# Optimization experiments

Measured on AMD Instinct MI355X. Metric: run time of the kernel, lower is better.

Reference implementation:

```python
import jax, jax.numpy as jnp
import numpy as np

B, C, D, H, W = 8, 256, 128, 64, 64


def setup_inputs() -> dict:
    key = jax.random.key(0)
    ks = jax.random.split(key, 7)
    s = 1.0 / np.sqrt(C)
    return {
        "q": jax.random.normal(ks[0], (B, C, H, W), dtype=jnp.float32),
        "k": jax.random.normal(ks[1], (B, C, H, W), dtype=jnp.float32),
        "v": jax.random.normal(ks[2], (B, C, H, W), dtype=jnp.float32),
        "W_theta": jax.random.normal(ks[3], (D, C), dtype=jnp.float32) * s,
        "W_phi": jax.random.normal(ks[4], (D, C), dtype=jnp.float32) * s,
        "W_g": jax.random.normal(ks[5], (D, C), dtype=jnp.float32) * s,
        "W_out": jax.random.normal(ks[6], (C, D), dtype=jnp.float32) * (1.0 / np.sqrt(D)),
    }


def reference(q, k, v, W_theta, W_phi, W_g, W_out):
    # 1x1 conv projections (no bias) == channel matmuls
    b, c, h, w = q.shape
    d = W_theta.shape[0]
    n = h * w
    qp = jnp.einsum('bchw,dc->bhwd', q, W_theta).reshape(b, n, d)   # [B,N,d]
    kp = jnp.einsum('bchw,dc->bhwd', k, W_phi).reshape(b, n, d)     # [B,N,d]
    vp = jnp.einsum('bchw,dc->bhwd', v, W_g).reshape(b, n, d)       # [B,N,d]
    # embedded_gaussian: scores / sqrt(d), softmax over dim=1 (query axis!)
    scores = jnp.einsum('bnd,bmd->bnm', qp, kp) / jnp.sqrt(jnp.asarray(d, qp.dtype))
    attn = jax.nn.softmax(scores, axis=1)                           # NOTE: axis=1, matches torch dim=1
    out = jnp.einsum('bnm,bmd->bnd', attn, vp).reshape(b, h, w, d)  # [B,H,W,d]
    out = jnp.einsum('bhwd,cd->bchw', out, W_out)                   # conv_out 1x1
    return v + out
```

## Files before the change

### kernel.cpp

```cpp
#include <hip/hip_runtime.h>
#include <stdint.h>

#define B_ 8
#define C_ 256
#define D_ 128
#define N_ 4096

typedef __bf16 bf16x8 __attribute__((ext_vector_type(8)));
typedef uint16_t u16x8 __attribute__((ext_vector_type(8)));
typedef uint16_t u16x4 __attribute__((ext_vector_type(4)));
typedef float f32x4 __attribute__((ext_vector_type(4)));

__device__ inline uint16_t f2bf(float x) {
    union { float f; uint32_t u; } v; v.f = x;
    uint32_t u = v.u;
    return (uint16_t)((u + 0x7FFFu + ((u >> 16) & 1u)) >> 16);
}

__global__ __launch_bounds__(256) void prep_weights(
    const float* __restrict__ wt, const float* __restrict__ wp,
    const float* __restrict__ wg, const float* __restrict__ wo,
    uint16_t* __restrict__ bwt, uint16_t* __restrict__ bwp,
    uint16_t* __restrict__ bwg, uint16_t* __restrict__ bwo)
{
    int i = blockIdx.x * 256 + threadIdx.x;
    const float scale = 0.08838834764831845f;
    bwt[i] = f2bf(wt[i] * scale);
    bwp[i] = f2bf(wp[i]);
    bwg[i] = f2bf(wg[i]);
    bwo[i] = f2bf(wo[i]);
}

__global__ __launch_bounds__(256) void proj_kernel(
    const float* __restrict__ q, const float* __restrict__ k, const float* __restrict__ v,
    const uint16_t* __restrict__ bwt, const uint16_t* __restrict__ bwp, const uint16_t* __restrict__ bwg,
    uint16_t* __restrict__ qp, uint16_t* __restrict__ kp, uint16_t* __restrict__ vpT)
{
    const int which = blockIdx.z;
    const float* src = (which == 0) ? q : ((which == 1) ? k : v);
    const uint16_t* w = (which == 0) ? bwt : ((which == 1) ? bwp : bwg);
    const int b   = blockIdx.y;
    const int n0  = blockIdx.x * 64;
    const int wav = threadIdx.x >> 6;
    const int lane = threadIdx.x & 63;
    const int col = lane & 15;
    const int quad = lane >> 4;
    const int n = n0 + wav * 16 + col;

    const float* srcb = src + (size_t)b * C_ * N_;

    f32x4 acc[8];
#pragma unroll
    for (int mf = 0; mf < 8; ++mf) acc[mf] = (f32x4){0.f, 0.f, 0.f, 0.f};

    for (int kc = 0; kc < 8; ++kc) {
        const int cbase = kc * 32 + quad * 8;
        u16x8 bb;
#pragma unroll
        for (int j = 0; j < 8; ++j)
            bb[j] = f2bf(srcb[(size_t)(cbase + j) * N_ + n]);
        bf16x8 bfrag = __builtin_bit_cast(bf16x8, bb);
#pragma unroll
        for (int mf = 0; mf < 8; ++mf) {
            bf16x8 afrag = *(const bf16x8*)(w + (size_t)(mf * 16 + col) * C_ + cbase);
            acc[mf] = __builtin_amdgcn_mfma_f32_16x16x32_bf16(afrag, bfrag, acc[mf], 0, 0, 0);
        }
    }

    if (which < 2) {
        uint16_t* dst = (which == 0) ? qp : kp;
        uint16_t* base = dst + ((size_t)b * N_ + n) * D_;
#pragma unroll
        for (int mf = 0; mf < 8; ++mf) {
            u16x4 pk;
#pragma unroll
            for (int r = 0; r < 4; ++r) pk[r] = f2bf(acc[mf][r]);
            *(u16x4*)(base + mf * 16 + quad * 4) = pk;
        }
    } else {
        uint16_t* base = vpT + (size_t)b * D_ * N_;
#pragma unroll
        for (int mf = 0; mf < 8; ++mf)
#pragma unroll
            for (int r = 0; r < 4; ++r) {
                int d = mf * 16 + quad * 4 + r;
                base[(size_t)d * N_ + n] = f2bf(acc[mf][r]);
            }
    }
}

__global__ __launch_bounds__(256) void pass1_denom(
    const uint16_t* __restrict__ qp, const uint16_t* __restrict__ kp,
    float* __restrict__ inv_denom)
{
    const int b  = blockIdx.y;
    const int m0 = blockIdx.x * 64;
    const int wav = threadIdx.x >> 6;
    const int lane = threadIdx.x & 63;
    const int col = lane & 15;
    const int quad = lane >> 4;

    const uint16_t* qpb = qp + (size_t)b * N_ * D_;
    const uint16_t* kpb = kp + (size_t)b * N_ * D_;

    bf16x8 bfr[4][4];
#pragma unroll
    for (int mf = 0; mf < 4; ++mf)
#pragma unroll
        for (int kc = 0; kc < 4; ++kc)
            bfr[mf][kc] = *(const bf16x8*)(kpb + (size_t)(m0 + mf * 16 + col) * D_ + kc * 32 + quad * 8);

    float colsum[4] = {0.f, 0.f, 0.f, 0.f};

    for (int it = 0; it < 64; ++it) {
        const int nbase = it * 64 + wav * 16;
        bf16x8 afr[4];
#pragma unroll
        for (int kc = 0; kc < 4; ++kc)
            afr[kc] = *(const bf16x8*)(qpb + (size_t)(nbase + col) * D_ + kc * 32 + quad * 8);
#pragma unroll
        for (int mf = 0; mf < 4; ++mf) {
            f32x4 acc = (f32x4){0.f, 0.f, 0.f, 0.f};
#pragma unroll
            for (int kc = 0; kc < 4; ++kc)
                acc = __builtin_amdgcn_mfma_f32_16x16x32_bf16(afr[kc], bfr[mf][kc], acc, 0, 0, 0);
#pragma unroll
            for (int r = 0; r < 4; ++r)
                colsum[mf] += __expf(acc[r]);
        }
    }

    __shared__ float cs[4][64];
#pragma unroll
    for (int mf = 0; mf < 4; ++mf) {
        float s = colsum[mf];
        s += __shfl_down(s, 16, 64);
        s += __shfl_down(s, 32, 64);
        if (quad == 0) cs[wav][mf * 16 + col] = s;
    }
    __syncthreads();
    if (threadIdx.x < 64) {
        float s = cs[0][threadIdx.x] + cs[1][threadIdx.x] + cs[2][threadIdx.x] + cs[3][threadIdx.x];
        inv_denom[(size_t)b * N_ + m0 + threadIdx.x] = 1.0f / s;
    }
}

__global__ __launch_bounds__(256) void pass2_attn(
    const uint16_t* __restrict__ qp, const uint16_t* __restrict__ kp,
    const uint16_t* __restrict__ vpT, const float* __restrict__ inv_denom,
    uint16_t* __restrict__ obuf)
{
    const int b  = blockIdx.x & 7;
    const int n0 = (blockIdx.x >> 3) * 64;
    const int wav = threadIdx.x >> 6;
    const int lane = threadIdx.x & 63;
    const int col = lane & 15;
    const int quad = lane >> 4;

    const uint16_t* qpb = qp + (size_t)b * N_ * D_;
    const uint16_t* kpb = kp + (size_t)b * N_ * D_;
    const uint16_t* vtb = vpT + (size_t)b * D_ * N_;
    const float* invd = inv_denom + (size_t)b * N_;

    __shared__ __align__(16) uint16_t stage[2][16 * 512];
    __shared__ __align__(16) uint16_t plds_all[4][16][40];
    uint16_t (*plds)[40] = plds_all[wav];

    const uint16_t* kp_lane = kpb + (size_t)col * D_ + quad * 8;
    const uint16_t* vt_lane = vtb + (size_t)col * N_ + quad * 8;

#define STAGE(bufidx, m0_)                                                          \
    {                                                                               \
        uint16_t* lb = &stage[bufidx][0];                                           \
        _Pragma("unroll")                                                           \
        for (int j = 0; j < 4; ++j) {                                               \
            const int fid = wav * 4 + j;                                            \
            const uint16_t* g;                                                      \
            if (fid < 8)                                                            \
                g = kp_lane + (size_t)((m0_) + (fid >> 2) * 16) * D_ + (fid & 3) * 32; \
            else                                                                    \
                g = vt_lane + (size_t)((fid - 8) * 16) * N_ + (m0_);                \
            __builtin_amdgcn_global_load_lds(                                       \
                (const __attribute__((address_space(1))) unsigned int*)g,           \
                (__attribute__((address_space(3))) unsigned int*)(lb + fid * 512),  \
                16, 0, 0);                                                          \
        }                                                                           \
    }

    const int nrow = n0 + wav * 16 + col;
    bf16x8 qfr[4];
#pragma unroll
    for (int kc = 0; kc < 4; ++kc)
        qfr[kc] = *(const bf16x8*)(qpb + (size_t)nrow * D_ + kc * 32 + quad * 8);

    f32x4 oacc[8];
#pragma unroll
    for (int df = 0; df < 8; ++df) oacc[df] = (f32x4){0.f, 0.f, 0.f, 0.f};

    STAGE(0, 0);
    __syncthreads();

    for (int chunk = 0; chunk < N_ / 32; ++chunk) {
        const int m0 = chunk * 32;
        const int cur = chunk & 1;
        STAGE(cur ^ 1, (m0 + 32) & (N_ - 1));

        const uint16_t* sb = &stage[cur][0];
        f32x4 sacc0 = (f32x4){0.f, 0.f, 0.f, 0.f};
        f32x4 sacc1 = (f32x4){0.f, 0.f, 0.f, 0.f};
#pragma unroll
        for (int kc = 0; kc < 4; ++kc) {
            bf16x8 b0 = *(const bf16x8*)(sb + (size_t)kc * 512 + lane * 8);
            sacc0 = __builtin_amdgcn_mfma_f32_16x16x32_bf16(qfr[kc], b0, sacc0, 0, 0, 0);
        }
#pragma unroll
        for (int kc = 0; kc < 4; ++kc) {
            bf16x8 b1 = *(const bf16x8*)(sb + (size_t)(4 + kc) * 512 + lane * 8);
            sacc1 = __builtin_amdgcn_mfma_f32_16x16x32_bf16(qfr[kc], b1, sacc1, 0, 0, 0);
        }
        const float inv0 = invd[m0 + col];
        const float inv1 = invd[m0 + 16 + col];
#pragma unroll
        for (int r = 0; r < 4; ++r) {
            plds[quad * 4 + r][col]      = f2bf(__expf(sacc0[r]) * inv0);
            plds[quad * 4 + r][16 + col] = f2bf(__expf(sacc1[r]) * inv1);
        }
        bf16x8 pfrag = *(const bf16x8*)&plds[col][quad * 8];
#pragma unroll
        for (int df = 0; df < 8; ++df) {
            bf16x8 vfr = *(const bf16x8*)(sb + (size_t)(8 + df) * 512 + lane * 8);
            oacc[df] = __builtin_amdgcn_mfma_f32_16x16x32_bf16(pfrag, vfr, oacc[df], 0, 0, 0);
        }
        __syncthreads();
    }
#undef STAGE

    uint16_t* ob = obuf + ((size_t)b * N_ + n0 + wav * 16) * D_;
#pragma unroll
    for (int df = 0; df < 8; ++df)
#pragma unroll
        for (int r = 0; r < 4; ++r)
            ob[(size_t)(quad * 4 + r) * D_ + df * 16 + col] = f2bf(oacc[df][r]);
}

__global__ __launch_bounds__(256) void pass3_out(
    const uint16_t* __restrict__ obuf, const uint16_t* __restrict__ bwo,
    const float* __restrict__ v, float* __restrict__ out)
{
    const int b  = blockIdx.y;
    const int n0 = blockIdx.x * 64;
    const int wav = threadIdx.x >> 6;
    const int lane = threadIdx.x & 63;
    const int col = lane & 15;
    const int quad = lane >> 4;
    const int n = n0 + wav * 16 + col;

    const uint16_t* ob = obuf + (size_t)b * N_ * D_;
    const float* vb = v + (size_t)b * C_ * N_;
    float* outb = out + (size_t)b * C_ * N_;

    bf16x8 bfr[4];
#pragma unroll
    for (int kc = 0; kc < 4; ++kc)
        bfr[kc] = *(const bf16x8*)(ob + (size_t)n * D_ + kc * 32 + quad * 8);

#pragma unroll
    for (int cf = 0; cf < 16; ++cf) {
        f32x4 acc = (f32x4){0.f, 0.f, 0.f, 0.f};
#pragma unroll
        for (int kc = 0; kc < 4; ++kc) {
            bf16x8 afr = *(const bf16x8*)(bwo + (size_t)(cf * 16 + col) * D_ + kc * 32 + quad * 8);
            acc = __builtin_amdgcn_mfma_f32_16x16x32_bf16(afr, bfr[kc], acc, 0, 0, 0);
        }
#pragma unroll
        for (int r = 0; r < 4; ++r) {
            const int c = cf * 16 + quad * 4 + r;
            const size_t idx = (size_t)c * N_ + n;
            outb[idx] = vb[idx] + acc[r];
        }
    }
}

extern "C" void kernel_launch(void* const* d_in, const int* in_sizes, int n_in,
                              void* d_out, int out_size, void* d_ws, size_t ws_size,
                              hipStream_t stream) {
    const float* q  = (const float*)d_in[0];
    const float* k  = (const float*)d_in[1];
    const float* v  = (const float*)d_in[2];
    const float* wt = (const float*)d_in[3];
    const float* wp = (const float*)d_in[4];
    const float* wg = (const float*)d_in[5];
    const float* wo = (const float*)d_in[6];
    float* out = (float*)d_out;

    const size_t PROJ = (size_t)B_ * N_ * D_;
    uint16_t* qp   = (uint16_t*)d_ws;
    uint16_t* kp   = qp + PROJ;
    uint16_t* vpT  = kp + PROJ;
    uint16_t* obuf = vpT + PROJ;
    uint16_t* bwt  = obuf + PROJ;
    uint16_t* bwp  = bwt + (size_t)D_ * C_;
    uint16_t* bwg  = bwp + (size_t)D_ * C_;
    uint16_t* bwo  = bwg + (size_t)D_ * C_;
    float* invd    = (float*)(bwo + (size_t)D_ * C_);

    prep_weights<<<dim3(128), 256, 0, stream>>>(wt, wp, wg, wo, bwt, bwp, bwg, bwo);
    proj_kernel<<<dim3(N_ / 64, B_, 3), 256, 0, stream>>>(q, k, v, bwt, bwp, bwg, qp, kp, vpT);
    pass1_denom<<<dim3(N_ / 64, B_), 256, 0, stream>>>(qp, kp, invd);
    pass2_attn<<<dim3(512), 256, 0, stream>>>(qp, kp, vpT, invd, obuf);
    pass3_out<<<dim3(N_ / 64, B_), 256, 0, stream>>>(obuf, bwo, v, out);
}
```

Before: 431.9 us.

## Split attention key range across two blocks and fold log2e into scale

Pass 2 now splits the key dimension into two halves, launching twice as many blocks (1024 instead of 512). Each half writes a partial output buffer, and pass 3 sums the two buffers through extra MFMAs in the output projection. The theta scale now includes log2(e), so the exp becomes a native exp2. Pass 1 block indexing is interleaved by batch. The split is meant to fill the GPU's compute units better, at the cost of reloading Q and writing an extra partial buffer. Rounding each partial to bf16 adds a small precision loss.

Result: no change. 427.3 us (-1.1%).

```diff
diff --git a/kernel.cpp b/kernel.cpp
--- a/kernel.cpp
+++ b/kernel.cpp
@@ -16,6 +16,8 @@
     uint32_t u = v.u;
     return (uint16_t)((u + 0x7FFFu + ((u >> 16) & 1u)) >> 16);
 }
+
+__device__ inline float dexp2(float x) { return __builtin_amdgcn_exp2f(x); }
 
 __global__ __launch_bounds__(256) void prep_weights(
     const float* __restrict__ wt, const float* __restrict__ wp,
@@ -24,7 +26,7 @@
     uint16_t* __restrict__ bwg, uint16_t* __restrict__ bwo)
 {
     int i = blockIdx.x * 256 + threadIdx.x;
-    const float scale = 0.08838834764831845f;
+    const float scale = 0.127517431f;
     bwt[i] = f2bf(wt[i] * scale);
     bwp[i] = f2bf(wp[i]);
     bwg[i] = f2bf(wg[i]);
@@ -93,8 +95,8 @@
     const uint16_t* __restrict__ qp, const uint16_t* __restrict__ kp,
     float* __restrict__ inv_denom)
 {
-    const int b  = blockIdx.y;
-    const int m0 = blockIdx.x * 64;
+    const int b  = blockIdx.x & 7;
+    const int m0 = (blockIdx.x >> 3) * 64;
     const int wav = threadIdx.x >> 6;
     const int lane = threadIdx.x & 63;
     const int col = lane & 15;
@@ -126,7 +128,7 @@
                 acc = __builtin_amdgcn_mfma_f32_16x16x32_bf16(afr[kc], bfr[mf][kc], acc, 0, 0, 0);
 #pragma unroll
             for (int r = 0; r < 4; ++r)
-                colsum[mf] += __expf(acc[r]);
+                colsum[mf] += dexp2(acc[r]);
         }
     }
 
@@ -148,10 +150,11 @@
 __global__ __launch_bounds__(256) void pass2_attn(
     const uint16_t* __restrict__ qp, const uint16_t* __restrict__ kp,
     const uint16_t* __restrict__ vpT, const float* __restrict__ inv_denom,
-    uint16_t* __restrict__ obuf)
-{
-    const int b  = blockIdx.x & 7;
-    const int n0 = (blockIdx.x >> 3) * 64;
+    uint16_t* __restrict__ obuf0, uint16_t* __restrict__ obuf1)
+{
+    const int b    = blockIdx.x & 7;
+    const int half = (blockIdx.x >> 3) & 1;
+    const int n0   = (blockIdx.x >> 4) * 64;
     const int wav = threadIdx.x >> 6;
     const int lane = threadIdx.x & 63;
     const int col = lane & 15;
@@ -197,11 +200,12 @@
 #pragma unroll
     for (int df = 0; df < 8; ++df) oacc[df] = (f32x4){0.f, 0.f, 0.f, 0.f};
 
-    STAGE(0, 0);
+    const int mstart = half * (N_ / 2);
+    STAGE(0, mstart);
     __syncthreads();
 
-    for (int chunk = 0; chunk < N_ / 32; ++chunk) {
-        const int m0 = chunk * 32;
+    for (int chunk = 0; chunk < (N_ / 2) / 32; ++chunk) {
+        const int m0 = mstart + chunk * 32;
         const int cur = chunk & 1;
         STAGE(cur ^ 1, (m0 + 32) & (N_ - 1));
 
@@ -222,8 +226,8 @@
         const float inv1 = invd[m0 + 16 + col];
 #pragma unroll
         for (int r = 0; r < 4; ++r) {
-            plds[quad * 4 + r][col]      = f2bf(__expf(sacc0[r]) * inv0);
-            plds[quad * 4 + r][16 + col] = f2bf(__expf(sacc1[r]) * inv1);
+            plds[quad * 4 + r][col]      = f2bf(dexp2(sacc0[r]) * inv0);
+            plds[quad * 4 + r][16 + col] = f2bf(dexp2(sacc1[r]) * inv1);
         }
         bf16x8 pfrag = *(const bf16x8*)&plds[col][quad * 8];
 #pragma unroll
@@ -235,7 +239,8 @@
     }
 #undef STAGE
 
-    uint16_t* ob = obuf + ((size_t)b * N_ + n0 + wav * 16) * D_;
+    uint16_t* obufH = half ? obuf1 : obuf0;
+    uint16_t* ob = obufH + ((size_t)b * N_ + n0 + wav * 16) * D_;
 #pragma unroll
     for (int df = 0; df < 8; ++df)
 #pragma unroll
@@ -244,7 +249,8 @@
 }
 
 __global__ __launch_bounds__(256) void pass3_out(
-    const uint16_t* __restrict__ obuf, const uint16_t* __restrict__ bwo,
+    const uint16_t* __restrict__ obuf0, const uint16_t* __restrict__ obuf1,
+    const uint16_t* __restrict__ bwo,
     const float* __restrict__ v, float* __restrict__ out)
 {
     const int b  = blockIdx.y;
@@ -255,14 +261,17 @@
     const int quad = lane >> 4;
     const int n = n0 + wav * 16 + col;
 
-    const uint16_t* ob = obuf + (size_t)b * N_ * D_;
+    const uint16_t* ob0 = obuf0 + (size_t)b * N_ * D_;
+    const uint16_t* ob1 = obuf1 + (size_t)b * N_ * D_;
     const float* vb = v + (size_t)b * C_ * N_;
     float* outb = out + (size_t)b * C_ * N_;
 
-    bf16x8 bfr[4];
-#pragma unroll
-    for (int kc = 0; kc < 4; ++kc)
-        bfr[kc] = *(const bf16x8*)(ob + (size_t)n * D_ + kc * 32 + quad * 8);
+    bf16x8 bfr0[4], bfr1[4];
+#pragma unroll
+    for (int kc = 0; kc < 4; ++kc) {
+        bfr0[kc] = *(const bf16x8*)(ob0 + (size_t)n * D_ + kc * 32 + quad * 8);
+        bfr1[kc] = *(const bf16x8*)(ob1 + (size_t)n * D_ + kc * 32 + quad * 8);
+    }
 
 #pragma unroll
     for (int cf = 0; cf < 16; ++cf) {
@@ -270,7 +279,8 @@
 #pragma unroll
         for (int kc = 0; kc < 4; ++kc) {
             bf16x8 afr = *(const bf16x8*)(bwo + (size_t)(cf * 16 + col) * D_ + kc * 32 + quad * 8);
-            acc = __builtin_amdgcn_mfma_f32_16x16x32_bf16(afr, bfr[kc], acc, 0, 0, 0);
+            acc = __builtin_amdgcn_mfma_f32_16x16x32_bf16(afr, bfr0[kc], acc, 0, 0, 0);
+            acc = __builtin_amdgcn_mfma_f32_16x16x32_bf16(afr, bfr1[kc], acc, 0, 0, 0);
         }
 #pragma unroll
         for (int r = 0; r < 4; ++r) {
@@ -294,19 +304,20 @@
     float* out = (float*)d_out;
 
     const size_t PROJ = (size_t)B_ * N_ * D_;
-    uint16_t* qp   = (uint16_t*)d_ws;
-    uint16_t* kp   = qp + PROJ;
-    uint16_t* vpT  = kp + PROJ;
-    uint16_t* obuf = vpT + PROJ;
-    uint16_t* bwt  = obuf + PROJ;
-    uint16_t* bwp  = bwt + (size_t)D_ * C_;
-    uint16_t* bwg  = bwp + (size_t)D_ * C_;
-    uint16_t* bwo  = bwg + (size_t)D_ * C_;
-    float* invd    = (float*)(bwo + (size_t)D_ * C_);
+    uint16_t* qp    = (uint16_t*)d_ws;
+    uint16_t* kp    = qp + PROJ;
+    uint16_t* vpT   = kp + PROJ;
+    uint16_t* obuf0 = vpT + PROJ;
+    uint16_t* bwt   = obuf0 + PROJ;
+    uint16_t* bwp   = bwt + (size_t)D_ * C_;
+    uint16_t* bwg   = bwp + (size_t)D_ * C_;
+    uint16_t* bwo   = bwg + (size_t)D_ * C_;
+    float* invd     = (float*)(bwo + (size_t)D_ * C_);
+    uint16_t* obuf1 = (uint16_t*)(invd + (size_t)B_ * N_);
 
     prep_weights<<<dim3(128), 256, 0, stream>>>(wt, wp, wg, wo, bwt, bwp, bwg, bwo);
     proj_kernel<<<dim3(N_ / 64, B_, 3), 256, 0, stream>>>(q, k, v, bwt, bwp, bwg, qp, kp, vpT);
-    pass1_denom<<<dim3(N_ / 64, B_), 256, 0, stream>>>(qp, kp, invd);
-    pass2_attn<<<dim3(512), 256, 0, stream>>>(qp, kp, vpT, invd, obuf);
-    pass3_out<<<dim3(N_ / 64, B_), 256, 0, stream>>>(obuf, bwo, v, out);
-}
+    pass1_denom<<<dim3(512), 256, 0, stream>>>(qp, kp, invd);
+    pass2_attn<<<dim3(1024), 256, 0, stream>>>(qp, kp, vpT, invd, obuf0, obuf1);
+    pass3_out<<<dim3(N_ / 64, B_), 256, 0, stream>>>(obuf0, obuf1, bwo, v, out);
+}
```
